# Performance work log

Measured on AMD Instinct MI355X. Metric: run time of the kernel, lower is better.

The kernel has to match this reference:

```python
import jax, jax.numpy as jnp
import numpy as np

K = 3
PADDING = 1
STRIDE = 1


def _unfold(x, k, padding, stride):
    """torch.nn.Unfold(k, dilation=1, padding, stride) on NCHW input.
    Returns [B, C*k*k, L] with channel ordering (C, kh, kw), matching torch."""
    patches = jax.lax.conv_general_dilated_patches(
        x,
        filter_shape=(k, k),
        window_strides=(stride, stride),
        padding=[(padding, padding), (padding, padding)],
    )  # [B, C*k*k, H', W'], channels ordered (C, kh, kw)
    B, CK2, Hp, Wp = patches.shape
    return patches.reshape(B, CK2, Hp * Wp)


def setup_inputs() -> dict:
    key = jax.random.key(0)
    k1, k2 = jax.random.split(key)
    key_map = jax.random.normal(k1, (8, 256, 64, 64), dtype=jnp.float32)
    query_map = jax.random.normal(k2, (8, 256, 64, 64), dtype=jnp.float32)
    return {"key_map": key_map, "query_map": query_map}


def reference(key_map, query_map):
    k = K
    B, C = key_map.shape[0], key_map.shape[1]
    key_uf = _unfold(key_map, k, PADDING, STRIDE)      # [B, C*k*k, L]
    query_uf = _unfold(query_map, k, PADDING, STRIDE)  # [B, C*k*k, L]
    # torch .view(B, C, -1, k*k): raw contiguous reshape of [B, C*k*k, L]
    # -> [B, C, L, k*k] (note: this interleaves the (k*k, L) block, exactly
    # as the original contiguous view does).
    key_uf = key_uf.reshape(B, C, -1, key_uf.shape[-2] // C)
    query_uf = query_uf.reshape(B, C, -1, query_uf.shape[-2] // C)
    center = k * k // 2
    return key_uf * query_uf[:, :, :, center:center + 1]
```

## Files before the change

kernel.cpp:

```cpp
#include <hip/hip_runtime.h>

typedef unsigned int uint_t;

#define HW        4096
#define CHUNKS_PER_BC 4608
#define NBLOCKS   36864

static __device__ __forceinline__ float qload(const float* __restrict__ qplane, int l2) {
    int idx = l2 * 9 + 4;
    int j4  = idx >> 12;
    int l4  = idx & 4095;
    int h4  = l4 >> 6;
    int w4  = l4 & 63;
    int jd  = (j4 * 11) >> 5;
    int hh  = h4 + jd - 1;
    int ww  = w4 + (j4 - jd * 3) - 1;
    if ((unsigned)hh < 64u && (unsigned)ww < 64u)
        return qplane[(hh << 6) + ww];
    return 0.0f;
}

__global__ __launch_bounds__(256) void appcomp_kernel(
    const float* __restrict__ key,
    const float* __restrict__ query,
    float* __restrict__ out)
{
    int g  = blockIdx.x * 256 + threadIdx.x;
    int bc = g / CHUNKS_PER_BC;
    int t  = g - bc * CHUNKS_PER_BC;
    int r  = t << 3;
    int j  = r >> 12;
    int l  = r & 4095;
    int h  = l >> 6;
    int w0 = l & 63;

    int jd3 = (j * 11) >> 5;
    int dh  = jd3 - 1;
    int dw  = j - jd3 * 3 - 1;
    int hh  = h + dh;

    const float* kplane = key + bc * HW;

    float kf[8];
    if ((unsigned)hh < 64u) {
        const float* rowp = kplane + (hh << 6);
        float4 a = *(const float4*)(rowp + w0);
        float4 b = *(const float4*)(rowp + w0 + 4);
        float e[8] = {a.x, a.y, a.z, a.w, b.x, b.y, b.z, b.w};
        if (dw == 0) {
            #pragma unroll
            for (int i = 0; i < 8; i++) kf[i] = e[i];
        } else if (dw < 0) {
            kf[0] = (w0 > 0) ? rowp[w0 - 1] : 0.0f;
            #pragma unroll
            for (int i = 1; i < 8; i++) kf[i] = e[i - 1];
        } else {
            #pragma unroll
            for (int i = 0; i < 7; i++) kf[i] = e[i + 1];
            kf[7] = (w0 < 56) ? rowp[w0 + 8] : 0.0f;
        }
    } else {
        #pragma unroll
        for (int i = 0; i < 8; i++) kf[i] = 0.0f;
    }

    int l2a   = r / 9;
    int m9    = r - l2a * 9;
    int split = 9 - m9;
    const float* qplane = query + bc * HW;
    float qa = qload(qplane, l2a);
    float qb = (split < 8) ? qload(qplane, l2a + 1) : 0.0f;

    float f[8];
    #pragma unroll
    for (int i = 0; i < 8; i++) {
        float q = (i < split) ? qa : qb;
        f[i] = kf[i] * q;
    }

    float* op = out + (size_t)g * 8;
    *(float4*)(op)     = make_float4(f[0], f[1], f[2], f[3]);
    *(float4*)(op + 4) = make_float4(f[4], f[5], f[6], f[7]);
}

extern "C" void kernel_launch(void* const* d_in, const int* in_sizes, int n_in,
                              void* d_out, int out_size, void* d_ws, size_t ws_size,
                              hipStream_t stream) {
    const float* key   = (const float*)d_in[0];
    const float* query = (const float*)d_in[1];
    float* out = (float*)d_out;
    appcomp_kernel<<<NBLOCKS, 256, 0, stream>>>(key, query, out);
}
```

Measured before the change: 394.7 us.

## Stage key and query planes in LDS with one block per channel plane

Each block now handles one (batch, channel) plane. It loads the full 64x64 key and query planes into shared memory, then loops 18 times to produce that plane's 36864 outputs, reading shifted key values and gathered query centers from LDS instead of global memory. This removes redundant global/L2 reads of the same plane across many blocks. In exchange the grid drops to 2048 blocks with 32KB LDS each, which can lower occupancy and adds a barrier before compute. The kernel is dominated by output writes, so the gain from fewer reads may be small.

```diff
diff --git a/kernel.cpp b/kernel.cpp
--- a/kernel.cpp
+++ b/kernel.cpp
@@ -1,12 +1,8 @@
 #include <hip/hip_runtime.h>
 
-typedef unsigned int uint_t;
+#define HW 4096
 
-#define HW        4096
-#define CHUNKS_PER_BC 4608
-#define NBLOCKS   36864
-
-static __device__ __forceinline__ float qload(const float* __restrict__ qplane, int l2) {
+static __device__ __forceinline__ float qload_lds(const float* q_s, int l2) {
     int idx = l2 * 9 + 4;
     int j4  = idx >> 12;
     int l4  = idx & 4095;
@@ -16,7 +12,7 @@
     int hh  = h4 + jd - 1;
     int ww  = w4 + (j4 - jd * 3) - 1;
     if ((unsigned)hh < 64u && (unsigned)ww < 64u)
-        return qplane[(hh << 6) + ww];
+        return q_s[(hh << 6) + ww];
     return 0.0f;
 }
 
@@ -25,62 +21,78 @@
     const float* __restrict__ query,
     float* __restrict__ out)
 {
-    int g  = blockIdx.x * 256 + threadIdx.x;
-    int bc = g / CHUNKS_PER_BC;
-    int t  = g - bc * CHUNKS_PER_BC;
-    int r  = t << 3;
-    int j  = r >> 12;
-    int l  = r & 4095;
-    int h  = l >> 6;
-    int w0 = l & 63;
+    __shared__ float k_s[HW];
+    __shared__ float q_s[HW];
 
-    int jd3 = (j * 11) >> 5;
-    int dh  = jd3 - 1;
-    int dw  = j - jd3 * 3 - 1;
-    int hh  = h + dh;
+    const int bc  = blockIdx.x;
+    const int tid = threadIdx.x;
 
-    const float* kplane = key + bc * HW;
+    {
+        const float4* kg = (const float4*)(key + bc * HW);
+        const float4* qg = (const float4*)(query + bc * HW);
+        float4* k4 = (float4*)k_s;
+        float4* q4 = (float4*)q_s;
+        #pragma unroll
+        for (int i = 0; i < 4; i++) {
+            int idx = i * 256 + tid;
+            k4[idx] = kg[idx];
+            q4[idx] = qg[idx];
+        }
+    }
+    __syncthreads();
 
-    float kf[8];
-    if ((unsigned)hh < 64u) {
-        const float* rowp = kplane + (hh << 6);
-        float4 a = *(const float4*)(rowp + w0);
-        float4 b = *(const float4*)(rowp + w0 + 4);
-        float e[8] = {a.x, a.y, a.z, a.w, b.x, b.y, b.z, b.w};
-        if (dw == 0) {
-            #pragma unroll
-            for (int i = 0; i < 8; i++) kf[i] = e[i];
-        } else if (dw < 0) {
-            kf[0] = (w0 > 0) ? rowp[w0 - 1] : 0.0f;
-            #pragma unroll
-            for (int i = 1; i < 8; i++) kf[i] = e[i - 1];
+    float* oplane = out + (size_t)bc * 36864;
+    for (int i = 0; i < 18; i++) {
+        int t  = i * 256 + tid;
+        int r  = t << 3;
+        int j  = r >> 12;
+        int l  = r & 4095;
+        int h  = l >> 6;
+        int w0 = l & 63;
+
+        int jd3 = (j * 11) >> 5;
+        int dh  = jd3 - 1;
+        int dw  = j - jd3 * 3 - 1;
+        int hh  = h + dh;
+
+        float kf[8];
+        if ((unsigned)hh < 64u) {
+            const float* rowp = k_s + (hh << 6);
+            float4 a = *(const float4*)(rowp + w0);
+            float4 b = *(const float4*)(rowp + w0 + 4);
+            float e[8] = {a.x, a.y, a.z, a.w, b.x, b.y, b.z, b.w};
+            if (dw == 0) {
+                #pragma unroll
+                for (int q = 0; q < 8; q++) kf[q] = e[q];
+            } else if (dw < 0) {
+                kf[0] = (w0 > 0) ? rowp[w0 - 1] : 0.0f;
+                #pragma unroll
+                for (int q = 1; q < 8; q++) kf[q] = e[q - 1];
+            } else {
+                #pragma unroll
+                for (int q = 0; q < 7; q++) kf[q] = e[q + 1];
+                kf[7] = (w0 < 56) ? rowp[w0 + 8] : 0.0f;
+            }
         } else {
             #pragma unroll
-            for (int i = 0; i < 7; i++) kf[i] = e[i + 1];
-            kf[7] = (w0 < 56) ? rowp[w0 + 8] : 0.0f;
+            for (int q = 0; q < 8; q++) kf[q] = 0.0f;
         }
-    } else {
+
+        int l2a   = r / 9;
+        int m9    = r - l2a * 9;
+        int split = 9 - m9;
+        float qa = qload_lds(q_s, l2a);
+        float qb = (split < 8) ? qload_lds(q_s, l2a + 1) : 0.0f;
+
+        float f[8];
         #pragma unroll
-        for (int i = 0; i < 8; i++) kf[i] = 0.0f;
+        for (int q = 0; q < 8; q++)
+            f[q] = kf[q] * ((q < split) ? qa : qb);
+
+        float* op = oplane + r;
+        *(float4*)(op)     = make_float4(f[0], f[1], f[2], f[3]);
+        *(float4*)(op + 4) = make_float4(f[4], f[5], f[6], f[7]);
     }
-
-    int l2a   = r / 9;
-    int m9    = r - l2a * 9;
-    int split = 9 - m9;
-    const float* qplane = query + bc * HW;
-    float qa = qload(qplane, l2a);
-    float qb = (split < 8) ? qload(qplane, l2a + 1) : 0.0f;
-
-    float f[8];
-    #pragma unroll
-    for (int i = 0; i < 8; i++) {
-        float q = (i < split) ? qa : qb;
-        f[i] = kf[i] * q;
-    }
-
-    float* op = out + (size_t)g * 8;
-    *(float4*)(op)     = make_float4(f[0], f[1], f[2], f[3]);
-    *(float4*)(op + 4) = make_float4(f[4], f[5], f[6], f[7]);
 }
 
 extern "C" void kernel_launch(void* const* d_in, const int* in_sizes, int n_in,
@@ -89,5 +101,5 @@
     const float* key   = (const float*)d_in[0];
     const float* query = (const float*)d_in[1];
     float* out = (float*)d_out;
-    appcomp_kernel<<<NBLOCKS, 256, 0, stream>>>(key, query, out);
+    appcomp_kernel<<<2048, 256, 0, stream>>>(key, query, out);
 }
```

New measurement: 356.4 us. -9.7%, faster.
